# Optimization experiments

Measured on AMD Instinct MI355X. Metric: run time of the kernel, lower is better.

The kernel has to match this reference:

```python
import jax, jax.numpy as jnp
import numpy as np

N_GRAPH = 100000
N_CAND = 1000
N_EDGES = 3200000
F_IN = 32


def _param(k, shape):
    return jax.random.normal(k, shape, dtype=jnp.float32) * 0.1


def setup_inputs() -> dict:
    key = jax.random.key(0)
    ks = jax.random.split(key, 20)
    inp = {
        "x": jax.random.normal(ks[0], (N_GRAPH, F_IN), dtype=jnp.float32),
        "candidate_set": jax.random.normal(ks[1], (N_CAND, F_IN), dtype=jnp.float32),
        "edge_index": jax.random.randint(ks[2], (2, N_EDGES), 0, N_GRAPH, dtype=jnp.int32),
        # GCN stack 32 -> 16 -> 24 -> 32
        "W1": _param(ks[3], (F_IN, 16)), "b1": jnp.zeros((16,), jnp.float32),
        "W2": _param(ks[4], (16, 24)),   "b2": jnp.zeros((24,), jnp.float32),
        "W3": _param(ks[5], (24, 32)),   "b3": jnp.zeros((32,), jnp.float32),
        # start-node MLP: 32 -> 16 -> 1
        "Ws1": _param(ks[6], (32, 16)), "bs1": jnp.zeros((16,), jnp.float32),
        "Ws2": _param(ks[7], (16, 1)),  "bs2": jnp.zeros((1,), jnp.float32),
        # end-node MLP: 32 -> 24 -> 1
        "We1": _param(ks[8], (32, 24)), "be1": jnp.zeros((24,), jnp.float32),
        "We2": _param(ks[9], (24, 1)),  "be2": jnp.zeros((1,), jnp.float32),
    }
    return inp


def _relu6(v):
    return jnp.clip(v, 0.0, 6.0)


def _gcn(h, row, col, dinv, W, b, N):
    # PyG GCNConv: h @ W, then D^-1/2 (A+I) D^-1/2 aggregation, then + bias
    h = h @ W
    norm = (dinv[row] * dinv[col])[:, None]
    return jax.ops.segment_sum(h[row] * norm, col, num_segments=N) + b


def reference(x, candidate_set, edge_index, W1, b1, W2, b2, W3, b3,
              Ws1, bs1, Ws2, bs2, We1, be1, We2, be2):
    n_graph = x.shape[0]
    h = jnp.concatenate([x, candidate_set], axis=0)  # [N, F_IN]
    N = h.shape[0]
    sl = jnp.arange(N, dtype=edge_index.dtype)
    row = jnp.concatenate([edge_index[0], sl])  # self-loops appended
    col = jnp.concatenate([edge_index[1], sl])
    deg = jax.ops.segment_sum(jnp.ones(row.shape[0], h.dtype), col, num_segments=N)
    dinv = 1.0 / jnp.sqrt(deg)  # deg >= 1 thanks to self-loops

    for W, b in ((W1, b1), (W2, b2), (W3, b3)):
        h = _gcn(h, row, col, dinv, W, b, N)  # [N, 32] at the end

    # start-node head: softmax over nodes (dim 0)
    start_probs = jax.nn.softmax(_relu6(h @ Ws1 + bs1) @ Ws2 + bs2, axis=0)  # [N,1]
    mask = jnp.ones_like(start_probs).at[n_graph:].set(0.0)  # zero out candidates
    start_probs = start_probs * mask
    start_probs = jnp.where(start_probs == 0.0, 1e-10, start_probs)
    start_probs = start_probs.squeeze()  # [N]
    start_node = jax.random.categorical(jax.random.key(42), jnp.log(start_probs))

    # end-node head
    end_probs = jax.nn.softmax(_relu6(h @ We1 + be1) @ We2 + be2, axis=0)  # [N,1]
    end_probs = end_probs.at[start_node].set(0.0)
    end_probs = jnp.where(end_probs == 0.0, 1e-10, end_probs)
    end_probs = end_probs.squeeze()  # [N]
    end_node = jax.random.categorical(jax.random.key(43), jnp.log(end_probs))

    new_edge = jnp.stack([start_node, end_node]).astype(edge_index.dtype)[:, None]
    edge_index_new = jnp.concatenate([edge_index, new_edge], axis=1)
    return (h, start_probs, end_probs, start_node, end_node, edge_index_new)
```

## Files before the change

### kernel.cpp

```cpp
#include <hip/hip_runtime.h>
#include <math.h>

#define TPB 256
#define BNODES 256
#define EPB 8192
#define SENT (-1)
#define MAXBKT 512
#define STAGE_CAP 9472
#define PMS 3200

typedef _Float16 h8 __attribute__((ext_vector_type(8)));
typedef _Float16 hf;


__device__ __forceinline__ float jax_gumbel(unsigned key, unsigned i) {
  unsigned x0 = 0u, x1 = i;
  unsigned ks0 = 0u, ks1 = key, ks2 = key ^ 0x1BD11BDAu;
  x0 += ks0; x1 += ks1;
#define TFR(r) { x0 += x1; x1 = (x1 << (r)) | (x1 >> (32 - (r))); x1 ^= x0; }
  TFR(13) TFR(15) TFR(26) TFR(6)
  x0 += ks1; x1 += ks2 + 1u;
  TFR(17) TFR(29) TFR(16) TFR(24)
  x0 += ks2; x1 += ks0 + 2u;
  TFR(13) TFR(15) TFR(26) TFR(6)
  x0 += ks0; x1 += ks1 + 3u;
  TFR(17) TFR(29) TFR(16) TFR(24)
  x0 += ks1; x1 += ks2 + 4u;
  TFR(13) TFR(15) TFR(26) TFR(6)
  x0 += ks2; x1 += ks0 + 5u;
#undef TFR
  unsigned bits = x0 ^ x1;
  float f = __uint_as_float((bits >> 9) | 0x3f800000u) - 1.0f;
  float u = (f == 0.0f) ? 1.17549435e-38f : f;
  return -logf(-logf(u));
}

__global__ void prep_k(const float* __restrict__ W2, const float* __restrict__ W3,
                       const float* __restrict__ b1, const float* __restrict__ b2,
                       float* __restrict__ W23, float* __restrict__ bvA, float* __restrict__ bvB,
                       int* __restrict__ breal, int nbkt) {
  int t = threadIdx.x;
  for (int i = t; i < nbkt; i += TPB) breal[i] = 0;
  for (int idx = t; idx < 512; idx += TPB) {
    int i = idx >> 5, j = idx & 31;
    float s = 0.f;
    for (int k = 0; k < 24; k++) s += W2[i * 24 + k] * W3[k * 32 + j];
    W23[idx] = s;
  }
  __syncthreads();
  if (t < 32) {
    float sA = 0.f;
    for (int i = 0; i < 16; i++) sA += b1[i] * W23[i * 32 + t];
    bvA[t] = sA;
    float sB = 0.f;
    for (int k = 0; k < 24; k++) sB += b2[k] * W3[k * 32 + t];
    bvB[t] = sB;
  }
}

__global__ void hist2_k(const int* __restrict__ col, int* __restrict__ breal,
                        int ne, int nbkt) {
  __shared__ int h[MAXBKT];
  int t = threadIdx.x;
  for (int i = t; i < nbkt; i += TPB) h[i] = 0;
  __syncthreads();
  int base = blockIdx.x * EPB;
#pragma unroll
  for (int k = 0; k < EPB / TPB; k++) {
    int idx = base + k * TPB + t;
    if (idx < ne) atomicAdd(&h[col[idx] >> 8], 1);
  }
  __syncthreads();
  for (int i = t; i < nbkt; i += TPB) if (h[i]) atomicAdd(&breal[i], h[i]);
}

__global__ void sbase_k(const int* __restrict__ breal, int* __restrict__ rbase,
                        int* __restrict__ base, int* __restrict__ cursor,
                        int nbkt, int nblk) {
  __shared__ int sr[TPB], sp[TPB];
  int t = threadIdx.x;
  int vr[2], vp[2]; int tr = 0, tp = 0;
#pragma unroll
  for (int k = 0; k < 2; k++) {
    int i = t * 2 + k; int R = 0, P = 0;
    if (i < nbkt) {
      R = breal[i];
      int mn = (nblk < R) ? nblk : R;
      P = (R + 3 * mn + 15) & ~15;
    }
    vr[k] = R; vp[k] = P; tr += R; tp += P;
  }
  sr[t] = tr; sp[t] = tp; __syncthreads();
  for (int off = 1; off < TPB; off <<= 1) {
    int ar = (t >= off) ? sr[t - off] : 0;
    int ap = (t >= off) ? sp[t - off] : 0;
    __syncthreads();
    sr[t] += ar; sp[t] += ap;
    __syncthreads();
  }
  int er = sr[t] - tr, ep = sp[t] - tp;
#pragma unroll
  for (int k = 0; k < 2; k++) {
    int i = t * 2 + k;
    if (i < nbkt) { rbase[i] = er; base[i] = ep; cursor[i] = ep; }
    er += vr[k]; ep += vp[k];
  }
}

__global__ void __launch_bounds__(TPB, 1)
scat_k(const int* __restrict__ row, const int* __restrict__ col,
       int* __restrict__ cursor, int* __restrict__ pairs,
       float* __restrict__ e0, float* __restrict__ e1,
       int ne, int nbkt) {
  __shared__ int sbase[MAXBKT], lofs[MAXBKT], lcur[MAXBKT], lsz[MAXBKT];
  __shared__ int ssc[TPB];
  __shared__ int stage[STAGE_CAP];
  int t = threadIdx.x;
  int b = blockIdx.x;
  for (int i = t; i < nbkt; i += TPB) lsz[i] = 0;
  __syncthreads();
  int base0 = b * EPB;
#pragma unroll
  for (int k = 0; k < EPB / TPB; k++) {
    int idx = base0 + k * TPB + t;
    if (idx < ne) atomicAdd(&lsz[col[idx] >> 8], 1);
  }
  __syncthreads();
  int i0 = 2 * t, i1 = 2 * t + 1;
  int L0 = (i0 < nbkt) ? lsz[i0] : 0, L1 = (i1 < nbkt) ? lsz[i1] : 0;
  int P0 = (L0 + 3) & ~3, P1 = (L1 + 3) & ~3;
  int s = P0 + P1;
  ssc[t] = s; __syncthreads();
  for (int off = 1; off < TPB; off <<= 1) {
    int a = (t >= off) ? ssc[t - off] : 0;
    __syncthreads();
    ssc[t] += a;
    __syncthreads();
  }
  int excl = ssc[t] - s;
  if (i0 < nbkt) { lofs[i0] = excl; lcur[i0] = excl; if (L0) sbase[i0] = atomicAdd(&cursor[i0], P0); }
  if (i1 < nbkt) { lofs[i1] = excl + P0; lcur[i1] = excl + P0; if (L1) sbase[i1] = atomicAdd(&cursor[i1], P1); }
  __syncthreads();
#pragma unroll
  for (int k = 0; k < EPB / TPB; k++) {
    int idx = base0 + k * TPB + t;
    if (idx < ne) {
      int c = col[idx];
      int r = row[idx];
      int p = atomicAdd(&lcur[c >> 8], 1);
      stage[p] = (r << 8) | (c & 255);
      e0[idx] = (float)r;
      e1[idx] = (float)c;
    }
  }
  __syncthreads();
  for (int i = t; i < nbkt; i += TPB) {
    int en = lofs[i] + lsz[i], pe = lofs[i] + ((lsz[i] + 3) & ~3);
    for (int p = en; p < pe; p++) stage[p] = SENT;
  }
  __syncthreads();
  int4* gp = (int4*)pairs;
  const int4* sp = (const int4*)stage;
  for (int i = t; i < nbkt; i += TPB) {
    int L = lsz[i]; if (!L) continue;
    int gb = sbase[i] >> 2, lb = lofs[i] >> 2, m = ((L + 3) & ~3) >> 2;
    for (int q = 0; q < m; q++) gp[gb + q] = sp[lb + q];
  }
}

__global__ void bbuild_k(const int* __restrict__ pairs, const int* __restrict__ base,
                         const int* __restrict__ cursor, const int* __restrict__ rbase,
                         int* __restrict__ rp, float* __restrict__ dinv,
                         int* __restrict__ csr, int n, int ne) {
  int bkt = blockIdx.x;
  int lo = bkt << 8;
  int t = threadIdx.x;
  int pstart = base[bkt];
  int pend   = cursor[bkt];
  int rbase_ = rbase[bkt];
  __shared__ int cnt[BNODES], sc[BNODES], pos[BNODES];
  cnt[t] = 0; __syncthreads();
  for (int p = pstart + t; p < pend; p += TPB) {
    int e = pairs[p];
    if (e >= 0) atomicAdd(&cnt[e & 255], 1);
  }
  __syncthreads();
  int own = cnt[t];
  sc[t] = own; __syncthreads();
  for (int off = 1; off < BNODES; off <<= 1) {
    int add = (t >= off) ? sc[t - off] : 0;
    __syncthreads();
    sc[t] += add;
    __syncthreads();
  }
  int excl = sc[t] - own;
  if (lo + t < n) {
    rp[lo + t] = rbase_ + excl;
    dinv[lo + t] = 1.0f / sqrtf((float)(own + 1));
  }
  pos[t] = rbase_ + excl;
  __syncthreads();
  for (int p = pstart + t; p < pend; p += TPB) {
    int e = pairs[p];
    if (e >= 0) {
      int q = atomicAdd(&pos[e & 255], 1);
      csr[q] = e >> 8;
    }
  }
  if (bkt == 0 && t == 0) rp[n] = ne;
}

__global__ void gemm16h_k(const float* __restrict__ A, const float* __restrict__ A2, int nsplit,
                          const float* __restrict__ W, const float* __restrict__ dinv,
                          hf* __restrict__ out, int n) {
  constexpr int FIN = 32, FOUT = 16, FP = 16;
  constexpr int NODES = TPB / FP;
  __shared__ float Ws[FIN * FOUT];
  __shared__ float Hs[NODES * (FIN + 1)];
  int t = threadIdx.x;
  int base = blockIdx.x * NODES;
  for (int i = t; i < FIN * FOUT; i += TPB) Ws[i] = W[i];
  for (int i = t; i < NODES * FIN; i += TPB) {
    int nl = i / FIN, k = i - nl * FIN;
    int g = base + nl;
    float v = 0.f;
    if (g < n) v = (g < nsplit) ? A[(size_t)g * FIN + k] : A2[(size_t)(g - nsplit) * FIN + k];
    Hs[nl * (FIN + 1) + k] = v;
  }
  __syncthreads();
  int nl = t / FP, j = t % FP;
  int g = base + nl;
  if (g < n) {
    float acc = 0.f;
#pragma unroll
    for (int k = 0; k < FIN; k++) acc += Hs[nl * (FIN + 1) + k] * Ws[k * FOUT + j];
    out[(size_t)g * FOUT + j] = (hf)(acc * dinv[g]);
  }
}

__global__ void agghs_k(const h8* __restrict__ ts, const int* __restrict__ csr,
                        const int* __restrict__ rp, const float* __restrict__ dinv,
                        const float* __restrict__ sin_, float* __restrict__ u_out,
                        float* __restrict__ us_out, h8* __restrict__ outv, int n) {
  int wave = blockIdx.x * (TPB / 64) + (threadIdx.x >> 6);
  int lane = threadIdx.x & 63;
  int j = lane & 1;
  int grp = (lane >> 1) & 3;
  int nl = lane >> 3;
  int c = wave * 8 + nl;
  bool valid = (c < n);
  float acc[8] = {0.f, 0.f, 0.f, 0.f, 0.f, 0.f, 0.f, 0.f};
  float accS = 0.f;
  if (valid) {
    int s = rp[c], e = rp[c + 1];
    int ch0 = s >> 2, ch1 = (e + 3) >> 2;
    int nch = ch1 - ch0;
    int k0 = ch0 + ((nch * grp) >> 2);
    int k1 = ch0 + ((nch * (grp + 1)) >> 2);
    for (int ch = k0; ch < k1; ch++) {
      int base = ch << 2;
      int4 e4 = *(const int4*)(csr + base);
      bool b0 = (base     >= s) & (base     < e);
      bool b1 = (base + 1 >= s) & (base + 1 < e);
      bool b2 = (base + 2 >= s) & (base + 2 < e);
      bool b3 = (base + 3 >= s) & (base + 3 < e);
      int r0 = b0 ? e4.x : 0;
      int r1 = b1 ? e4.y : 0;
      int r2 = b2 ? e4.z : 0;
      int r3 = b3 ? e4.w : 0;
      float m0 = b0 ? 1.f : 0.f, m1 = b1 ? 1.f : 0.f;
      float m2 = b2 ? 1.f : 0.f, m3 = b3 ? 1.f : 0.f;
      h8 v0 = ts[(r0 << 1) | j];
      h8 v1 = ts[(r1 << 1) | j];
      h8 v2 = ts[(r2 << 1) | j];
      h8 v3 = ts[(r3 << 1) | j];
      float sA = sin_[j ? r2 : r0];
      float sB = sin_[j ? r3 : r1];
      accS += sA * (j ? m2 : m0) + sB * (j ? m3 : m1);
#pragma unroll
      for (int k = 0; k < 8; k++)
        acc[k] += m0 * (float)v0[k] + m1 * (float)v1[k] + m2 * (float)v2[k] + m3 * (float)v3[k];
    }
  }
  accS += __shfl_xor(accS, 1, 64);
#pragma unroll
  for (int off = 2; off <= 4; off <<= 1) {
#pragma unroll
    for (int k = 0; k < 8; k++) acc[k] += __shfl_xor(acc[k], off, 64);
    accS += __shfl_xor(accS, off, 64);
  }
  if (valid && grp == 0) {
    h8 self = ts[(c << 1) | j];
    float d = dinv[c];
    float scl = d * d;
    h8 o;
#pragma unroll
    for (int k = 0; k < 8; k++) o[k] = (hf)(scl * (acc[k] + (float)self[k]));
    outv[(c << 1) | j] = o;
    if (j == 0) {
      float u = d * (accS + sin_[c]);
      u_out[c] = u;
      if (us_out) us_out[c] = u * d;
    }
  }
}

__global__ void agghch_k(const h8* __restrict__ ts, const int* __restrict__ csr,
                         const int* __restrict__ rp, const float* __restrict__ dinv,
                         const float* __restrict__ a1, const float* __restrict__ a2,
                         const float* __restrict__ W23, const float* __restrict__ bvA,
                         const float* __restrict__ bvB, const float* __restrict__ b3,
                         const float* __restrict__ Ws1, const float* __restrict__ bs1,
                         const float* __restrict__ ws2, const float* __restrict__ bs2,
                         const float* __restrict__ We1, const float* __restrict__ be1,
                         const float* __restrict__ we2, const float* __restrict__ be2,
                         float* __restrict__ out, float* __restrict__ slog,
                         float* __restrict__ elog, float* __restrict__ pm, int n) {
  __shared__ float Ws[512], vA[32], vB[32], vb[32];
  __shared__ float t3s[32][17];
  __shared__ float h3s[32][33];
  __shared__ float W1s[512], W2s[768], b1s[16], b2s[24], v1s[16], v2s[24], sb2[2];
  __shared__ float sm1[32], su1[32], sm2[32], su2[32];
  int t = threadIdx.x;
  for (int i = t; i < 512; i += TPB) { Ws[i] = W23[i]; W1s[i] = Ws1[i]; }
  for (int i = t; i < 768; i += TPB) W2s[i] = We1[i];
  if (t < 32) { vA[t] = bvA[t]; vB[t] = bvB[t]; vb[t] = b3[t]; }
  if (t < 16) { b1s[t] = bs1[t]; v1s[t] = ws2[t]; }
  if (t < 24) { b2s[t] = be1[t]; v2s[t] = we2[t]; }
  if (t == 0) { sb2[0] = bs2[0]; sb2[1] = be2[0]; }
  int wave = t >> 6;
  int lane = t & 63;
  int j = lane & 1;
  int grp = (lane >> 1) & 3;
  int nl = lane >> 3;
  int nlb = wave * 8 + nl;
  int c = blockIdx.x * 32 + nlb;
  bool valid = (c < n);
  float acc[8] = {0.f, 0.f, 0.f, 0.f, 0.f, 0.f, 0.f, 0.f};
  if (valid) {
    int s = rp[c], e = rp[c + 1];
    int ch0 = s >> 2, ch1 = (e + 3) >> 2;
    int nch = ch1 - ch0;
    int k0 = ch0 + ((nch * grp) >> 2);
    int k1 = ch0 + ((nch * (grp + 1)) >> 2);
    for (int ch = k0; ch < k1; ch++) {
      int base = ch << 2;
      int4 e4 = *(const int4*)(csr + base);
      bool b0 = (base     >= s) & (base     < e);
      bool b1 = (base + 1 >= s) & (base + 1 < e);
      bool b2 = (base + 2 >= s) & (base + 2 < e);
      bool b3b = (base + 3 >= s) & (base + 3 < e);
      int r0 = b0 ? e4.x : 0;
      int r1 = b1 ? e4.y : 0;
      int r2 = b2 ? e4.z : 0;
      int r3 = b3b ? e4.w : 0;
      float m0 = b0 ? 1.f : 0.f, m1 = b1 ? 1.f : 0.f;
      float m2 = b2 ? 1.f : 0.f, m3 = b3b ? 1.f : 0.f;
      h8 v0 = ts[(r0 << 1) | j];
      h8 v1 = ts[(r1 << 1) | j];
      h8 v2 = ts[(r2 << 1) | j];
      h8 v3 = ts[(r3 << 1) | j];
#pragma unroll
      for (int k = 0; k < 8; k++)
        acc[k] += m0 * (float)v0[k] + m1 * (float)v1[k] + m2 * (float)v2[k] + m3 * (float)v3[k];
    }
  }
#pragma unroll
  for (int off = 2; off <= 4; off <<= 1) {
#pragma unroll
    for (int k = 0; k < 8; k++) acc[k] += __shfl_xor(acc[k], off, 64);
  }
  if (valid && grp == 0) {
    h8 self = ts[(c << 1) | j];
    float d = dinv[c];
#pragma unroll
    for (int k = 0; k < 8; k++) t3s[nlb][j * 8 + k] = d * (acc[k] + (float)self[k]);
  }
  __syncthreads();
  int n2 = t >> 3, jb = t & 7;
  int g = blockIdx.x * 32 + n2;
  if (g < n) {
    float av = a1[g], bv = a2[g];
#pragma unroll
    for (int q = 0; q < 4; q++) {
      int j2 = jb + q * 8;
      float acc2 = 0.f;
#pragma unroll
      for (int k = 0; k < 16; k++) acc2 += t3s[n2][k] * Ws[k * 32 + j2];
      float hv = acc2 + bv * vA[j2] + av * vB[j2] + vb[j2];
      out[(size_t)g * 32 + j2] = hv;
      h3s[n2][j2] = hv;
    }
  }
  __syncthreads();
  float sP = 0.f, eP = 0.f;
  if (g < n) {
#pragma unroll
    for (int jj = 0; jj < 16; jj += 8) {
      int jh = jj + jb;
      float a = b1s[jh];
#pragma unroll
      for (int k = 0; k < 32; k++) a += h3s[n2][k] * W1s[k * 16 + jh];
      a = fminf(fmaxf(a, 0.f), 6.f);
      sP += a * v1s[jh];
    }
#pragma unroll
    for (int jj = 0; jj < 24; jj += 8) {
      int jh = jj + jb;
      float a = b2s[jh];
#pragma unroll
      for (int k = 0; k < 32; k++) a += h3s[n2][k] * W2s[k * 24 + jh];
      a = fminf(fmaxf(a, 0.f), 6.f);
      eP += a * v2s[jh];
    }
  }
#pragma unroll
  for (int off = 1; off <= 4; off <<= 1) {
    sP += __shfl_xor(sP, off, 64);
    eP += __shfl_xor(eP, off, 64);
  }
  if (jb == 0) {
    float s = -3.402823466e+38f, e2 = -3.402823466e+38f, w = 0.f;
    if (g < n) {
      s = sP + sb2[0]; e2 = eP + sb2[1]; w = 1.f;
      slog[g] = s; elog[g] = e2;
    }
    sm1[n2] = s;  su1[n2] = w;
    sm2[n2] = e2; su2[n2] = w;
  }
  __syncthreads();
  for (int st = 16; st > 0; st >>= 1) {
    if (t < st) {
      float M = fmaxf(sm1[t], sm1[t + st]);
      su1[t] = su1[t] * expf(sm1[t] - M) + su1[t + st] * expf(sm1[t + st] - M);
      sm1[t] = M;
      float M2 = fmaxf(sm2[t], sm2[t + st]);
      su2[t] = su2[t] * expf(sm2[t] - M2) + su2[t + st] * expf(sm2[t + st] - M2);
      sm2[t] = M2;
    }
    __syncthreads();
  }
  if (t == 0) {
    pm[blockIdx.x] = sm1[0]; pm[PMS + blockIdx.x] = su1[0];
    pm[2 * PMS + blockIdx.x] = sm2[0]; pm[3 * PMS + blockIdx.x] = su2[0];
  }
}

template <int HEAD>
__global__ void pargmax_k(const float* __restrict__ logit, const float* __restrict__ pm, int nb,
                          const float* __restrict__ sval, const int* __restrict__ sidx,
                          float* __restrict__ outp, unsigned key, int n, int ngraph,
                          float* __restrict__ pval, int* __restrict__ pidx,
                          float* __restrict__ dnode) {
  int t = threadIdx.x;
  __shared__ float smM[TPB], smS[TPB];
  __shared__ float sv0[TPB]; __shared__ int si0[TPB];
  const float* pmM = pm + (HEAD ? 2 * PMS : 0);
  const float* pmS = pm + (HEAD ? 3 * PMS : PMS);
  float m = -3.402823466e+38f, s0 = 0.f;
  for (int i = t; i < nb; i += TPB) {
    float bm = pmM[i], bs = pmS[i];
    float M = fmaxf(m, bm);
    s0 = s0 * expf(m - M) + bs * expf(bm - M); m = M;
  }
  smM[t] = m; smS[t] = s0; __syncthreads();
  for (int st = 128; st > 0; st >>= 1) {
    if (t < st) {
      float M = fmaxf(smM[t], smM[t + st]);
      smS[t] = smS[t] * expf(smM[t] - M) + smS[t + st] * expf(smM[t + st] - M);
      smM[t] = M;
    }
    __syncthreads();
  }
  float mx = smM[0], sm = smS[0];
  int ban = -1;
  if (HEAD) {
    sv0[t] = sval[t]; si0[t] = sidx[t]; __syncthreads();
    for (int st = 128; st > 0; st >>= 1) {
      if (t < st) {
        float v2 = sv0[t + st]; int i2 = si0[t + st];
        if (v2 > sv0[t] || (v2 == sv0[t] && i2 < si0[t])) { sv0[t] = v2; si0[t] = i2; }
      }
      __syncthreads();
    }
    ban = si0[0];
    if (blockIdx.x == 0 && t == 0) dnode[0] = (float)ban;
  }
  float bv = -3.402823466e+38f;
  int bi = 0x7fffffff;
  for (int i = blockIdx.x * TPB + t; i < n; i += gridDim.x * TPB) {
    float p = expf(logit[i] - mx) / sm;
    if (HEAD == 0) { if (i >= ngraph) p = 0.f; }
    else           { if (i == ban) p = 0.f; }
    if (p == 0.f) p = 1e-10f;
    outp[i] = p;
    float v = logf(p) + jax_gumbel(key, (unsigned)i);
    if (v > bv) { bv = v; bi = i; }
  }
  __shared__ float sv[TPB]; __shared__ int si[TPB];
  sv[t] = bv; si[t] = bi; __syncthreads();
  for (int st = 128; st > 0; st >>= 1) {
    if (t < st) {
      float v2 = sv[t + st]; int i2 = si[t + st];
      if (v2 > sv[t] || (v2 == sv[t] && i2 < si[t])) { sv[t] = v2; si[t] = i2; }
    }
    __syncthreads();
  }
  if (t == 0) { pval[blockIdx.x] = sv[0]; pidx[blockIdx.x] = si[0]; }
}

__global__ void argmax_fin_end_k(const float* pval, const int* pidx, int nb,
                                 const float* dstart, float* p_end, float* p_e0, float* p_e1) {
  int t = threadIdx.x;
  float bv = (t < nb) ? pval[t] : -3.402823466e+38f;
  int bi = (t < nb) ? pidx[t] : 0x7fffffff;
  __shared__ float sv[TPB]; __shared__ int si[TPB];
  sv[t] = bv; si[t] = bi; __syncthreads();
  for (int st = 128; st > 0; st >>= 1) {
    if (t < st) {
      float v2 = sv[t + st]; int i2 = si[t + st];
      if (v2 > sv[t] || (v2 == sv[t] && i2 < si[t])) { sv[t] = v2; si[t] = i2; }
    }
    __syncthreads();
  }
  if (t == 0) {
    int en = si[0];
    p_end[0] = (float)en;
    p_e0[0] = dstart[0];
    p_e1[0] = (float)en;
  }
}

extern "C" void kernel_launch(void* const* d_in, const int* in_sizes, int n_in,
                              void* d_out, int out_size, void* d_ws, size_t ws_size,
                              hipStream_t stream) {
  const float* x    = (const float*)d_in[0];
  const float* cand = (const float*)d_in[1];
  const int*   ei   = (const int*)d_in[2];
  const float* W1 = (const float*)d_in[3];  const float* b1  = (const float*)d_in[4];
  const float* W2 = (const float*)d_in[5];  const float* b2  = (const float*)d_in[6];
  const float* W3 = (const float*)d_in[7];  const float* b3  = (const float*)d_in[8];
  const float* Ws1= (const float*)d_in[9];  const float* bs1 = (const float*)d_in[10];
  const float* Ws2= (const float*)d_in[11]; const float* bs2 = (const float*)d_in[12];
  const float* We1= (const float*)d_in[13]; const float* be1 = (const float*)d_in[14];
  const float* We2= (const float*)d_in[15]; const float* be2 = (const float*)d_in[16];

  const int nG = in_sizes[0] / 32, nC = in_sizes[1] / 32;
  const int n  = nG + nC;
  const int ne = in_sizes[2] / 2;

  float* out = (float*)d_out;
  const size_t OFF1 = (size_t)n * 32;
  const size_t OFF2 = OFF1 + n;
  const size_t OFF3 = OFF2 + n;
  const size_t OFF4 = OFF3 + 1;
  const size_t OFF5 = OFF4 + 1;

  const int NBKT = (n + BNODES - 1) / BNODES;
  const int NBLK = (ne + EPB - 1) / EPB;

  float* wf = (float*)d_ws;
  int*   wi = (int*)d_ws;
  size_t NP = (((size_t)n + 2) + 63) & ~(size_t)63;
  size_t o = 0;
  int*   rp    = wi + o; o += NP;
  int*   breal = wi + o; o += 512;
  int*   rbase = wi + o; o += 512;
  int*   bbase = wi + o; o += 512;
  int*   bcur  = wi + o; o += 512;
  float* dinv  = wf + o; o += NP;
  float* a1v   = wf + o; o += NP;
  float* a1s   = wf + o; o += NP;
  float* a2v   = wf + o; o += NP;
  float* w23   = wf + o; o += 512;
  float* bvA   = wf + o; o += 64;
  float* bvB   = wf + o; o += 64;
  float* slogv = wf + o; o += NP;
  float* elogv = wf + o; o += NP;
  float* pmA   = wf + o; o += 4 * PMS;
  float* aval  = wf + o; o += 512;
  int*   aidx  = wi + o; o += 512;
  hf*    hh0   = (hf*)(wf + o); o += (size_t)n * 8 + 64;
  hf*    hh1   = (hf*)(wf + o); o += (size_t)n * 8 + 64;
  int*   csr   = wi + o; o += (size_t)ne + 64;
  int*   pairs = wi + o; o += (size_t)ne + 700000;

  const int* row = ei;
  const int* col = ei + ne;

  prep_k<<<1, TPB, 0, stream>>>(W2, W3, b1, b2, w23, bvA, bvB, breal, NBKT);
  hist2_k<<<NBLK, TPB, 0, stream>>>(col, breal, ne, NBKT);
  sbase_k<<<1, TPB, 0, stream>>>(breal, rbase, bbase, bcur, NBKT, NBLK);
  scat_k<<<NBLK, TPB, 0, stream>>>(row, col, bcur, pairs,
                                   out + OFF5, out + OFF5 + ne + 1, ne, NBKT);
  bbuild_k<<<NBKT, TPB, 0, stream>>>(pairs, bbase, bcur, rbase, rp, dinv, csr, n, ne);

  gemm16h_k<<<(n + 15) / 16, TPB, 0, stream>>>(x, cand, nG, W1, dinv, hh0, n);
  int gH = (n + 31) / 32;
  agghs_k<<<gH, TPB, 0, stream>>>((const h8*)hh0, csr, rp, dinv, dinv, a1v, a1s, (h8*)hh1, n);
  agghs_k<<<gH, TPB, 0, stream>>>((const h8*)hh1, csr, rp, dinv, a1s, a2v, nullptr, (h8*)hh0, n);
  agghch_k<<<gH, TPB, 0, stream>>>((const h8*)hh0, csr, rp, dinv, a1v, a2v,
                                   w23, bvA, bvB, b3,
                                   Ws1, bs1, Ws2, bs2, We1, be1, We2, be2,
                                   out, slogv, elogv, pmA, n);

  pargmax_k<0><<<256, TPB, 0, stream>>>(slogv, pmA, gH, nullptr, nullptr,
                                        out + OFF1, 42u, n, nG, aval, aidx, nullptr);

  pargmax_k<1><<<256, TPB, 0, stream>>>(elogv, pmA, gH, aval, aidx,
                                        out + OFF2, 43u, n, nG, aval + 256, aidx + 256,
                                        out + OFF3);
  argmax_fin_end_k<<<1, TPB, 0, stream>>>(aval + 256, aidx + 256, 256, out + OFF3,
                                          out + OFF4, out + OFF5 + ne, out + OFF5 + 2 * (size_t)ne + 1);
}
```

Baseline: 344.6 us.

## Replace bucketed two-pass CSR build with global atomic degree count and scatter

Replaces the bucketed CSR construction (per-block histogram, bucket scan, local staging into a padded pairs buffer, per-bucket build) with a plain approach: a global atomic degree count per node, a three-kernel prefix scan, and a scatter that uses a global atomic cursor per destination node. This drops the staging buffer and the bucket padding logic, but it issues 3.2M global atomics twice onto 100K addresses. The CSR neighbour order within each node also becomes nondeterministic, which only changes float summation order.

```diff
diff --git a/kernel.cpp b/kernel.cpp
--- a/kernel.cpp
+++ b/kernel.cpp
@@ -2,11 +2,6 @@
 #include <math.h>
 
 #define TPB 256
-#define BNODES 256
-#define EPB 8192
-#define SENT (-1)
-#define MAXBKT 512
-#define STAGE_CAP 9472
 #define PMS 3200
 
 typedef _Float16 h8 __attribute__((ext_vector_type(8)));
@@ -35,12 +30,15 @@
   return -logf(-logf(u));
 }
 
+__global__ void zero_k(int* __restrict__ deg, int n4) {
+  int i = blockIdx.x * TPB + threadIdx.x;
+  if (i < n4) ((int4*)deg)[i] = make_int4(0, 0, 0, 0);
+}
+
 __global__ void prep_k(const float* __restrict__ W2, const float* __restrict__ W3,
                        const float* __restrict__ b1, const float* __restrict__ b2,
-                       float* __restrict__ W23, float* __restrict__ bvA, float* __restrict__ bvB,
-                       int* __restrict__ breal, int nbkt) {
-  int t = threadIdx.x;
-  for (int i = t; i < nbkt; i += TPB) breal[i] = 0;
+                       float* __restrict__ W23, float* __restrict__ bvA, float* __restrict__ bvB) {
+  int t = threadIdx.x;
   for (int idx = t; idx < 512; idx += TPB) {
     int i = idx >> 5, j = idx & 31;
     float s = 0.f;
@@ -58,156 +56,92 @@
   }
 }
 
-__global__ void hist2_k(const int* __restrict__ col, int* __restrict__ breal,
-                        int ne, int nbkt) {
-  __shared__ int h[MAXBKT];
-  int t = threadIdx.x;
-  for (int i = t; i < nbkt; i += TPB) h[i] = 0;
-  __syncthreads();
-  int base = blockIdx.x * EPB;
-#pragma unroll
-  for (int k = 0; k < EPB / TPB; k++) {
-    int idx = base + k * TPB + t;
-    if (idx < ne) atomicAdd(&h[col[idx] >> 8], 1);
-  }
-  __syncthreads();
-  for (int i = t; i < nbkt; i += TPB) if (h[i]) atomicAdd(&breal[i], h[i]);
-}
-
-__global__ void sbase_k(const int* __restrict__ breal, int* __restrict__ rbase,
-                        int* __restrict__ base, int* __restrict__ cursor,
-                        int nbkt, int nblk) {
-  __shared__ int sr[TPB], sp[TPB];
-  int t = threadIdx.x;
-  int vr[2], vp[2]; int tr = 0, tp = 0;
-#pragma unroll
-  for (int k = 0; k < 2; k++) {
-    int i = t * 2 + k; int R = 0, P = 0;
-    if (i < nbkt) {
-      R = breal[i];
-      int mn = (nblk < R) ? nblk : R;
-      P = (R + 3 * mn + 15) & ~15;
-    }
-    vr[k] = R; vp[k] = P; tr += R; tp += P;
-  }
-  sr[t] = tr; sp[t] = tp; __syncthreads();
+__global__ void deg_k(const int* __restrict__ row, const int* __restrict__ col,
+                      int* __restrict__ deg, float* __restrict__ e0, float* __restrict__ e1,
+                      int ne) {
+  int stride = gridDim.x * TPB;
+  for (int i = blockIdx.x * TPB + threadIdx.x; i < ne; i += stride) {
+    int c = col[i];
+    int r = row[i];
+    atomicAdd(&deg[c], 1);
+    e0[i] = (float)r;
+    e1[i] = (float)c;
+  }
+}
+
+__global__ void scan1_k(const int* __restrict__ a, int* __restrict__ bsums, int n) {
+  int t = threadIdx.x;
+  int base = blockIdx.x * 1024 + t * 4;
+  int s = 0;
+#pragma unroll
+  for (int k = 0; k < 4; k++) { int i = base + k; if (i < n) s += a[i]; }
+  __shared__ int red[TPB];
+  red[t] = s; __syncthreads();
+  for (int st = 128; st > 0; st >>= 1) { if (t < st) red[t] += red[t + st]; __syncthreads(); }
+  if (t == 0) bsums[blockIdx.x] = red[0];
+}
+
+__global__ void scan_single_k(int* a, int m) {
+  __shared__ int sc[TPB];
+  int t = threadIdx.x;
+  int v[4]; int s = 0;
+#pragma unroll
+  for (int k = 0; k < 4; k++) { int i = t * 4 + k; v[k] = (i < m) ? a[i] : 0; s += v[k]; }
+  sc[t] = s; __syncthreads();
   for (int off = 1; off < TPB; off <<= 1) {
-    int ar = (t >= off) ? sr[t - off] : 0;
-    int ap = (t >= off) ? sp[t - off] : 0;
-    __syncthreads();
-    sr[t] += ar; sp[t] += ap;
-    __syncthreads();
-  }
-  int er = sr[t] - tr, ep = sp[t] - tp;
-#pragma unroll
-  for (int k = 0; k < 2; k++) {
-    int i = t * 2 + k;
-    if (i < nbkt) { rbase[i] = er; base[i] = ep; cursor[i] = ep; }
-    er += vr[k]; ep += vp[k];
-  }
-}
-
-__global__ void __launch_bounds__(TPB, 1)
-scat_k(const int* __restrict__ row, const int* __restrict__ col,
-       int* __restrict__ cursor, int* __restrict__ pairs,
-       float* __restrict__ e0, float* __restrict__ e1,
-       int ne, int nbkt) {
-  __shared__ int sbase[MAXBKT], lofs[MAXBKT], lcur[MAXBKT], lsz[MAXBKT];
-  __shared__ int ssc[TPB];
-  __shared__ int stage[STAGE_CAP];
-  int t = threadIdx.x;
-  int b = blockIdx.x;
-  for (int i = t; i < nbkt; i += TPB) lsz[i] = 0;
-  __syncthreads();
-  int base0 = b * EPB;
-#pragma unroll
-  for (int k = 0; k < EPB / TPB; k++) {
-    int idx = base0 + k * TPB + t;
-    if (idx < ne) atomicAdd(&lsz[col[idx] >> 8], 1);
-  }
-  __syncthreads();
-  int i0 = 2 * t, i1 = 2 * t + 1;
-  int L0 = (i0 < nbkt) ? lsz[i0] : 0, L1 = (i1 < nbkt) ? lsz[i1] : 0;
-  int P0 = (L0 + 3) & ~3, P1 = (L1 + 3) & ~3;
-  int s = P0 + P1;
-  ssc[t] = s; __syncthreads();
+    int add = (t >= off) ? sc[t - off] : 0;
+    __syncthreads();
+    sc[t] += add;
+    __syncthreads();
+  }
+  int excl = sc[t] - s;
+#pragma unroll
+  for (int k = 0; k < 4; k++) { int i = t * 4 + k; if (i < m) a[i] = excl; excl += v[k]; }
+  if (t == TPB - 1) a[m] = excl;
+}
+
+__global__ void scan3x_k(const int* __restrict__ deg, const int* __restrict__ bsums,
+                         int* __restrict__ rp, int* __restrict__ cursor,
+                         float* __restrict__ dinv, int n, int ne) {
+  int t = threadIdx.x;
+  int base = blockIdx.x * 1024 + t * 4;
+  int v[4]; int tsum = 0;
+#pragma unroll
+  for (int k = 0; k < 4; k++) {
+    int vv = (base + k < n) ? deg[base + k] : 0;
+    v[k] = vv; tsum += vv;
+  }
+  __shared__ int sc[TPB];
+  sc[t] = tsum; __syncthreads();
   for (int off = 1; off < TPB; off <<= 1) {
-    int a = (t >= off) ? ssc[t - off] : 0;
-    __syncthreads();
-    ssc[t] += a;
-    __syncthreads();
-  }
-  int excl = ssc[t] - s;
-  if (i0 < nbkt) { lofs[i0] = excl; lcur[i0] = excl; if (L0) sbase[i0] = atomicAdd(&cursor[i0], P0); }
-  if (i1 < nbkt) { lofs[i1] = excl + P0; lcur[i1] = excl + P0; if (L1) sbase[i1] = atomicAdd(&cursor[i1], P1); }
-  __syncthreads();
-#pragma unroll
-  for (int k = 0; k < EPB / TPB; k++) {
-    int idx = base0 + k * TPB + t;
-    if (idx < ne) {
-      int c = col[idx];
-      int r = row[idx];
-      int p = atomicAdd(&lcur[c >> 8], 1);
-      stage[p] = (r << 8) | (c & 255);
-      e0[idx] = (float)r;
-      e1[idx] = (float)c;
-    }
-  }
-  __syncthreads();
-  for (int i = t; i < nbkt; i += TPB) {
-    int en = lofs[i] + lsz[i], pe = lofs[i] + ((lsz[i] + 3) & ~3);
-    for (int p = en; p < pe; p++) stage[p] = SENT;
-  }
-  __syncthreads();
-  int4* gp = (int4*)pairs;
-  const int4* sp = (const int4*)stage;
-  for (int i = t; i < nbkt; i += TPB) {
-    int L = lsz[i]; if (!L) continue;
-    int gb = sbase[i] >> 2, lb = lofs[i] >> 2, m = ((L + 3) & ~3) >> 2;
-    for (int q = 0; q < m; q++) gp[gb + q] = sp[lb + q];
-  }
-}
-
-__global__ void bbuild_k(const int* __restrict__ pairs, const int* __restrict__ base,
-                         const int* __restrict__ cursor, const int* __restrict__ rbase,
-                         int* __restrict__ rp, float* __restrict__ dinv,
-                         int* __restrict__ csr, int n, int ne) {
-  int bkt = blockIdx.x;
-  int lo = bkt << 8;
-  int t = threadIdx.x;
-  int pstart = base[bkt];
-  int pend   = cursor[bkt];
-  int rbase_ = rbase[bkt];
-  __shared__ int cnt[BNODES], sc[BNODES], pos[BNODES];
-  cnt[t] = 0; __syncthreads();
-  for (int p = pstart + t; p < pend; p += TPB) {
-    int e = pairs[p];
-    if (e >= 0) atomicAdd(&cnt[e & 255], 1);
-  }
-  __syncthreads();
-  int own = cnt[t];
-  sc[t] = own; __syncthreads();
-  for (int off = 1; off < BNODES; off <<= 1) {
     int add = (t >= off) ? sc[t - off] : 0;
     __syncthreads();
     sc[t] += add;
     __syncthreads();
   }
-  int excl = sc[t] - own;
-  if (lo + t < n) {
-    rp[lo + t] = rbase_ + excl;
-    dinv[lo + t] = 1.0f / sqrtf((float)(own + 1));
-  }
-  pos[t] = rbase_ + excl;
-  __syncthreads();
-  for (int p = pstart + t; p < pend; p += TPB) {
-    int e = pairs[p];
-    if (e >= 0) {
-      int q = atomicAdd(&pos[e & 255], 1);
-      csr[q] = e >> 8;
-    }
-  }
-  if (bkt == 0 && t == 0) rp[n] = ne;
+  int excl = sc[t] - tsum + bsums[blockIdx.x];
+#pragma unroll
+  for (int k = 0; k < 4; k++) {
+    int i = base + k;
+    if (i < n) {
+      rp[i] = excl;
+      cursor[i] = excl;
+      dinv[i] = 1.0f / sqrtf((float)(v[k] + 1));
+    }
+    excl += v[k];
+  }
+  if (blockIdx.x == 0 && t == 0) rp[n] = ne;
+}
+
+__global__ void scat2_k(const int* __restrict__ row, const int* __restrict__ col,
+                        int* __restrict__ cursor, int* __restrict__ csr, int ne) {
+  int stride = gridDim.x * TPB;
+  for (int i = blockIdx.x * TPB + threadIdx.x; i < ne; i += stride) {
+    int c = col[i];
+    int r = row[i];
+    int q = atomicAdd(&cursor[c], 1);
+    csr[q] = r;
+  }
 }
 
 __global__ void gemm16h_k(const float* __restrict__ A, const float* __restrict__ A2, int nsplit,
@@ -556,18 +490,14 @@
   const size_t OFF4 = OFF3 + 1;
   const size_t OFF5 = OFF4 + 1;
 
-  const int NBKT = (n + BNODES - 1) / BNODES;
-  const int NBLK = (ne + EPB - 1) / EPB;
-
   float* wf = (float*)d_ws;
   int*   wi = (int*)d_ws;
   size_t NP = (((size_t)n + 2) + 63) & ~(size_t)63;
   size_t o = 0;
   int*   rp    = wi + o; o += NP;
-  int*   breal = wi + o; o += 512;
-  int*   rbase = wi + o; o += 512;
-  int*   bbase = wi + o; o += 512;
-  int*   bcur  = wi + o; o += 512;
+  int*   deg   = wi + o; o += NP;
+  int*   bcur  = wi + o; o += NP;
+  int*   bsums = wi + o; o += 384;
   float* dinv  = wf + o; o += NP;
   float* a1v   = wf + o; o += NP;
   float* a1s   = wf + o; o += NP;
@@ -582,18 +512,22 @@
   int*   aidx  = wi + o; o += 512;
   hf*    hh0   = (hf*)(wf + o); o += (size_t)n * 8 + 64;
   hf*    hh1   = (hf*)(wf + o); o += (size_t)n * 8 + 64;
+  o = (o + 3) & ~(size_t)3;
   int*   csr   = wi + o; o += (size_t)ne + 64;
-  int*   pairs = wi + o; o += (size_t)ne + 700000;
 
   const int* row = ei;
   const int* col = ei + ne;
 
-  prep_k<<<1, TPB, 0, stream>>>(W2, W3, b1, b2, w23, bvA, bvB, breal, NBKT);
-  hist2_k<<<NBLK, TPB, 0, stream>>>(col, breal, ne, NBKT);
-  sbase_k<<<1, TPB, 0, stream>>>(breal, rbase, bbase, bcur, NBKT, NBLK);
-  scat_k<<<NBLK, TPB, 0, stream>>>(row, col, bcur, pairs,
-                                   out + OFF5, out + OFF5 + ne + 1, ne, NBKT);
-  bbuild_k<<<NBKT, TPB, 0, stream>>>(pairs, bbase, bcur, rbase, rp, dinv, csr, n, ne);
+  const int nsc = (n + 1023) / 1024;
+  const int nz4 = (int)(NP >> 2);
+
+  zero_k<<<(nz4 + TPB - 1) / TPB, TPB, 0, stream>>>(deg, nz4);
+  prep_k<<<1, TPB, 0, stream>>>(W2, W3, b1, b2, w23, bvA, bvB);
+  deg_k<<<2048, TPB, 0, stream>>>(row, col, deg, out + OFF5, out + OFF5 + ne + 1, ne);
+  scan1_k<<<nsc, TPB, 0, stream>>>(deg, bsums, n);
+  scan_single_k<<<1, TPB, 0, stream>>>(bsums, nsc);
+  scan3x_k<<<nsc, TPB, 0, stream>>>(deg, bsums, rp, bcur, dinv, n, ne);
+  scat2_k<<<2048, TPB, 0, stream>>>(row, col, bcur, csr, ne);
 
   gemm16h_k<<<(n + 15) / 16, TPB, 0, stream>>>(x, cand, nG, W1, dinv, hh0, n);
   int gH = (n + 31) / 32;
```

After: 673.2 us. 1.95x slower.
